# Kernel optimization log

Hardware: AMD Instinct MI355X
Metric: run time of the kernel (lower is better)

## Reference

```python
import jax, jax.numpy as jnp
import numpy as np
import math

N = 512; D = 256; L = 6; H = 8; BINS = 64; LAM = 30.0; STEPS = 8; VOCAB = 20


def _pe(n, d):
    pos = jnp.arange(n, dtype=jnp.float32)[:, None]
    div = jnp.exp(jnp.arange(0, d, 2, dtype=jnp.float32) * (-math.log(10000.0) / d))
    pe = jnp.zeros((n, d), jnp.float32)
    pe = pe.at[:, 0::2].set(jnp.sin(pos * div))
    pe = pe.at[:, 1::2].set(jnp.cos(pos * div))
    return pe


def _ln(x, g, b, eps=1e-5):
    m = x.mean(-1, keepdims=True)
    v = x.var(-1, keepdims=True)
    return (x - m) / jnp.sqrt(v + eps) * g + b


def _gelu(x):
    return jax.nn.gelu(x, approximate=False)  # torch nn.GELU default (erf)


def setup_inputs() -> dict:
    key = jax.random.key(0)
    ks = jax.random.split(key, 20)
    s = 0.02
    nrm = lambda k, sh: jax.random.normal(k, sh, jnp.float32) * s
    z = lambda sh: jnp.zeros(sh, jnp.float32)
    o = lambda sh: jnp.ones(sh, jnp.float32)
    return {
        "tokens": jax.random.randint(ks[0], (1, N), 0, VOCAB),
        "emb": nrm(ks[1], (VOCAB, D)),
        "Wqkv": nrm(ks[2], (L, 3 * D, D)), "bqkv": z((L, 3 * D)),
        "Wo": nrm(ks[3], (L, D, D)), "bo": z((L, D)),
        "g1": o((L, D)), "be1": z((L, D)),
        "W1": nrm(ks[4], (L, 4 * D, D)), "b1": z((L, 4 * D)),
        "W2": nrm(ks[5], (L, D, 4 * D)), "b2": z((L, D)),
        "g2": o((L, D)), "be2": z((L, D)),
        "A1": nrm(ks[6], (D, D)), "a1b": z((D,)),
        "A2": nrm(ks[7], (1, D)), "a2b": z((1,)),
        "Cf": nrm(ks[8], (D, D)), "cb": z((D,)),
        "F1": nrm(ks[9], (D, 2 * D)), "f1b": z((D,)),
        "F2": nrm(ks[10], (BINS, D)), "f2b": z((BINS,)),
        "T1": nrm(ks[11], (D, D)), "t1b": z((D,)),
        "T2": nrm(ks[12], (2, D)), "t2b": z((2,)),
        "Cp": nrm(ks[13], (3, D)), "cpb": z((3,)),
        "noise": jax.random.normal(ks[14], (1, N, 3), jnp.float32),
    }


def reference(tokens, emb, Wqkv, bqkv, Wo, bo, g1, be1, W1, b1, W2, b2, g2, be2,
              A1, a1b, A2, a2b, Cf, cb, F1, f1b, F2, f2b, T1, t1b, T2, t2b,
              Cp, cpb, noise):
    x = emb[tokens] + _pe(N, D)  # [1,N,D]
    dh = D // H
    for l in range(L):  # post-norm TransformerEncoderLayer, ReLU activation
        qkv = x @ Wqkv[l].T + bqkv[l]  # [1,N,3D]
        q, k, v = jnp.split(qkv, 3, axis=-1)
        q = q.reshape(1, N, H, dh).transpose(0, 2, 1, 3)
        k = k.reshape(1, N, H, dh).transpose(0, 2, 1, 3)
        v = v.reshape(1, N, H, dh).transpose(0, 2, 1, 3)
        att = jax.nn.softmax(jnp.einsum('bhqd,bhkd->bhqk', q, k) / math.sqrt(dh), axis=-1)
        o = jnp.einsum('bhqk,bhkd->bhqd', att, v).transpose(0, 2, 1, 3).reshape(1, N, D)
        x = _ln(x + o @ Wo[l].T + bo[l], g1[l], be1[l])
        f = jax.nn.relu(x @ W1[l].T + b1[l]) @ W2[l].T + b2[l]
        x = _ln(x + f, g2[l], be2[l])
    latent = x
    # AdaptiveAlphaPredictor
    ah = _gelu(latent @ A1.T + a1b) @ A2.T + a2b  # [1,N,1]
    alpha = 1.2 + jax.nn.sigmoid(ah)[..., 0] * (3.5 - 1.2)  # [1,N]
    # CSOCRGAttention: power-law x exp-decay kernel over |i-j|
    idx = jnp.arange(N, dtype=jnp.float32)
    r = jnp.abs(idx[:, None] - idx[None, :]) + 1e-4  # [N,N]
    ap = (alpha[:, :, None] + alpha[:, None, :]) * 0.5  # [1,N,N]
    kern = r[None] ** (-ap) * jnp.exp(-r[None] / LAM)
    kern = kern / (kern.sum(-1, keepdims=True) + 1e-8)
    latent = jnp.einsum('bij,bjd->bid', kern, latent)
    # ContactPriorHead
    hh = latent @ Cf.T + cb
    contact = jax.nn.sigmoid(jnp.einsum('bid,bjd->bij', hh, hh))
    # DistogramHead: cat([xi, xj]) @ F1.T == xi @ F1[:, :D].T + xj @ F1[:, D:].T
    hi = latent @ F1[:, :D].T  # [1,N,D]
    hj = latent @ F1[:, D:].T  # [1,N,D]
    ph = _gelu(hi[:, :, None, :] + hj[:, None, :, :] + f1b)  # [1,N,N,D]
    disto = ph @ F2.T + f2b  # [1,N,N,BINS]
    # TorsionGenerator
    t = _gelu(latent @ T1.T + t1b) @ T2.T + t2b  # [1,N,2]
    phi = jnp.tanh(t[..., 0]) * jnp.pi
    psi = jnp.tanh(t[..., 1]) * jnp.pi
    # DiffusionInitializer: fixed small sequential refinement loop
    target = latent @ Cp.T + cpb  # [1,N,3]
    xc = noise
    for tt in reversed(range(STEPS)):
        a = (tt + 1) / STEPS
        xc = a * xc + (1.0 - a) * target
    return latent, alpha, contact, disto, phi, psi, xc


if __name__ == "__main__":
    outs = reference(**setup_inputs())
    for o in outs:
        print(o.shape, o.dtype)
```

## Files before the change

kernel.cpp:

```cpp
#include <hip/hip_runtime.h>
#include <hip/hip_bf16.h>

#define DEV __device__ __forceinline__

typedef float f32x4 __attribute__((ext_vector_type(4)));
typedef short short8 __attribute__((ext_vector_type(8)));
typedef short short4v __attribute__((ext_vector_type(4)));

#if __has_builtin(__builtin_amdgcn_exp2f)
#define EXP2F __builtin_amdgcn_exp2f
#else
#define EXP2F exp2f
#endif
#if __has_builtin(__builtin_amdgcn_rcpf)
#define RCPF __builtin_amdgcn_rcpf
#else
#define RCPF(x) (1.f / (x))
#endif

DEV short f2bf(float f) {
    union { float f; unsigned u; } c; c.f = f;
    unsigned r = (c.u + 0x7FFFu + ((c.u >> 16) & 1u)) >> 16;
    return (short)r;
}

DEV int cvt_pk_bf16(float lo, float hi) {
    int d;
    asm("v_cvt_pk_bf16_f32 %0, %1, %2" : "=v"(d) : "v"(lo), "v"(hi));
    return d;
}

DEV float gelu_fast(float x) {
    float x2 = x * x;
    float y = x * __builtin_fmaf(0.0356774081f, x2, 0.7978845608f);
    y = fminf(fmaxf(y, -15.f), 15.f);
    float e = EXP2F(y * 2.8853900817779268f);
    float r = RCPF(e + 1.f);
    float t = (e - 1.f) * r;
    return 0.5f * x * (1.f + t);
}

DEV float wred_sum(float v) {
    #pragma unroll
    for (int off = 1; off < 64; off <<= 1) v += __shfl_xor(v, off);
    return v;
}

struct CvtPack {
    const float* s[9];
    short* d[9];
    int n[9];
};
__global__ __launch_bounds__(256) void k_cvt_all(CvtPack p) {
    #pragma unroll 1
    for (int seg = 0; seg < 9; ++seg) {
        int n4 = p.n[seg] >> 2;
        const float4* src = (const float4*)p.s[seg];
        short4v* dst = (short4v*)p.d[seg];
        for (int i = blockIdx.x * 256 + threadIdx.x; i < n4; i += gridDim.x * 256) {
            float4 v = src[i];
            short4v o;
            o[0] = f2bf(v.x); o[1] = f2bf(v.y); o[2] = f2bf(v.z); o[3] = f2bf(v.w);
            dst[i] = o;
        }
    }
}

__global__ __launch_bounds__(256) void k_embed(const int* __restrict__ tokens,
                                               const float* __restrict__ emb,
                                               float* __restrict__ x,
                                               short* __restrict__ xb) {
    int n = blockIdx.x, d = threadIdx.x;
    int tok = tokens[n];
    float div = expf((float)((d >> 1) * 2) * -0.035977892079030837f);
    float arg = (float)n * div;
    float pe = (d & 1) ? cosf(arg) : sinf(arg);
    float v = emb[tok * 256 + d] + pe;
    x[n * 256 + d] = v;
    xb[n * 256 + d] = f2bf(v);
}

__global__ __launch_bounds__(64) void k_gemm16(const short* __restrict__ A,
                                               const short* __restrict__ W,
                                               const float* __restrict__ bias,
                                               float* __restrict__ outf,
                                               short* __restrict__ outb,
                                               short* __restrict__ vt,
                                               int M, int K, int ldw, int act) {
    int m0 = blockIdx.x * 16, n0 = blockIdx.y * 16;
    int lane = threadIdx.x;
    int cr = lane & 15, g = lane >> 4;
    const short* a0 = A + (size_t)(n0 + cr) * K + g * 8;
    const short* b0 = W + (size_t)(m0 + cr) * ldw + g * 8;
    f32x4 acc = {0.f, 0.f, 0.f, 0.f};
    #pragma unroll 8
    for (int k = 0; k < K; k += 32) {
        short8 av = *(const short8*)(a0 + k);
        short8 bv = *(const short8*)(b0 + k);
        acc = __builtin_amdgcn_mfma_f32_16x16x32_bf16(av, bv, acc, 0, 0, 0);
    }
    float bb = bias ? bias[m0 + cr] : 0.f;
    int m = m0 + cr;
    #pragma unroll
    for (int r = 0; r < 4; ++r) {
        int row = n0 + g * 4 + r;
        float v = acc[r] + bb;
        if (act == 1) v = fmaxf(v, 0.f);
        else if (act == 2) v = gelu_fast(v);
        else if (act == 3) v = 1.f / (1.f + __expf(-v));
        if (outf) outf[(size_t)row * M + m] = v;
        if (outb) outb[(size_t)row * M + m] = f2bf(v);
        if (vt && m >= 512) vt[(size_t)(m - 512) * 512 + row] = f2bf(v);
    }
}

__global__ __launch_bounds__(64) void k_attn3(const short* __restrict__ qkvb,
                                              const short* __restrict__ vt,
                                              short* __restrict__ obuf_bf) {
    __shared__ __align__(16) short Pb[16][40];
    int h = blockIdx.x, qt = blockIdx.y;
    int lane = threadIdx.x;
    int cr = lane & 15, g = lane >> 4;
    int qb = qt * 16;
    short8 qf = *(const short8*)(qkvb + (size_t)(qb + cr) * 768 + h * 32 + g * 8);
    f32x4 s[32];
    #pragma unroll
    for (int jt = 0; jt < 32; ++jt) {
        short8 kf = *(const short8*)(qkvb + (size_t)(jt * 16 + cr) * 768 + 256 + h * 32 + g * 8);
        f32x4 z = {0.f, 0.f, 0.f, 0.f};
        s[jt] = __builtin_amdgcn_mfma_f32_16x16x32_bf16(qf, kf, z, 0, 0, 0);
    }
    const float sc = 0.17677669529663687f;
    float m[4], l[4];
    #pragma unroll
    for (int r = 0; r < 4; ++r) {
        float mm = -1e30f;
        #pragma unroll
        for (int jt = 0; jt < 32; ++jt) mm = fmaxf(mm, s[jt][r]);
        #pragma unroll
        for (int off = 1; off < 16; off <<= 1) mm = fmaxf(mm, __shfl_xor(mm, off));
        m[r] = mm * sc;
    }
    #pragma unroll
    for (int r = 0; r < 4; ++r) {
        float ll = 0.f;
        #pragma unroll
        for (int jt = 0; jt < 32; ++jt) {
            float p = __expf(s[jt][r] * sc - m[r]);
            s[jt][r] = p;
            ll += p;
        }
        #pragma unroll
        for (int off = 1; off < 16; off <<= 1) ll += __shfl_xor(ll, off);
        l[r] = ll;
    }
    const short* vth0 = vt + (size_t)(h * 32 + cr) * 512;
    const short* vth1 = vt + (size_t)(h * 32 + 16 + cr) * 512;
    f32x4 o0 = {0.f,0.f,0.f,0.f}, o1 = o0;
    #pragma unroll
    for (int c = 0; c < 16; ++c) {
        #pragma unroll
        for (int r = 0; r < 4; ++r) {
            Pb[4 * g + r][cr]      = f2bf(s[2 * c][r]);
            Pb[4 * g + r][16 + cr] = f2bf(s[2 * c + 1][r]);
        }
        short8 pa = *(const short8*)&Pb[cr][g * 8];
        short8 v0 = *(const short8*)(vth0 + c * 32 + g * 8);
        short8 v1 = *(const short8*)(vth1 + c * 32 + g * 8);
        o0 = __builtin_amdgcn_mfma_f32_16x16x32_bf16(pa, v0, o0, 0, 0, 0);
        o1 = __builtin_amdgcn_mfma_f32_16x16x32_bf16(pa, v1, o1, 0, 0, 0);
    }
    #pragma unroll
    for (int r = 0; r < 4; ++r) {
        float inv = 1.f / l[r];
        int q = qb + 4 * g + r;
        short* op = obuf_bf + (size_t)q * 256 + h * 32;
        op[cr]      = f2bf(o0[r] * inv);
        op[16 + cr] = f2bf(o1[r] * inv);
    }
}

__global__ __launch_bounds__(64) void k_ln(const float* xr, const float* y,
                                           const float* __restrict__ g,
                                           const float* __restrict__ b,
                                           float* out, short* outb) {
    int n = blockIdx.x, lane = threadIdx.x;
    float4 xv = *(const float4*)(xr + (size_t)n * 256 + lane * 4);
    float4 yv = *(const float4*)(y + (size_t)n * 256 + lane * 4);
    float t0 = xv.x + yv.x, t1 = xv.y + yv.y, t2 = xv.z + yv.z, t3 = xv.w + yv.w;
    float s = t0 + t1 + t2 + t3;
    float sq = t0 * t0 + t1 * t1 + t2 * t2 + t3 * t3;
    s = wred_sum(s);
    sq = wred_sum(sq);
    float mean = s * (1.f / 256.f);
    float var = sq * (1.f / 256.f) - mean * mean;
    float rstd = rsqrtf(var + 1e-5f);
    float4 gv = *(const float4*)(g + lane * 4);
    float4 bv = *(const float4*)(b + lane * 4);
    float r0 = (t0 - mean) * rstd * gv.x + bv.x;
    float r1 = (t1 - mean) * rstd * gv.y + bv.y;
    float r2 = (t2 - mean) * rstd * gv.z + bv.z;
    float r3 = (t3 - mean) * rstd * gv.w + bv.w;
    *(float4*)(out + (size_t)n * 256 + lane * 4) = make_float4(r0, r1, r2, r3);
    short4v ob; ob[0] = f2bf(r0); ob[1] = f2bf(r1); ob[2] = f2bf(r2); ob[3] = f2bf(r3);
    *(short4v*)(outb + (size_t)n * 256 + lane * 4) = ob;
}

__global__ __launch_bounds__(64) void k_alpha(const float* __restrict__ g,
                                              const float* __restrict__ A2,
                                              const float* __restrict__ a2b,
                                              float* __restrict__ alpha) {
    int n = blockIdx.x, lane = threadIdx.x;
    float4 gv = *(const float4*)(g + (size_t)n * 256 + lane * 4);
    float4 av = *(const float4*)(A2 + lane * 4);
    float s = gv.x * av.x + gv.y * av.y + gv.z * av.z + gv.w * av.w;
    s = wred_sum(s);
    if (lane == 0) {
        float ah = s + a2b[0];
        alpha[n] = 1.2f + 2.3f / (1.f + __expf(-ah));
    }
}

__global__ __launch_bounds__(256) void k_kern(const float* __restrict__ latent,
                                              const float* __restrict__ alpha,
                                              float* __restrict__ out,
                                              short* __restrict__ outb) {
    __shared__ float wl[512];
    __shared__ float partial[4];
    int i = blockIdx.x, t = threadIdx.x;
    float ai = alpha[i];
    float w0, w1;
    {
        int j = t;
        float dd = fabsf((float)(i - j)) + 1e-4f;
        float ap = 0.5f * (ai + alpha[j]);
        w0 = exp2f(-ap * __log2f(dd) - dd * 0.048089834696298776f);
        j = t + 256;
        dd = fabsf((float)(i - j)) + 1e-4f;
        ap = 0.5f * (ai + alpha[j]);
        w1 = exp2f(-ap * __log2f(dd) - dd * 0.048089834696298776f);
    }
    wl[t] = w0; wl[t + 256] = w1;
    float s = wred_sum(w0 + w1);
    if ((t & 63) == 0) partial[t >> 6] = s;
    __syncthreads();
    float S = partial[0] + partial[1] + partial[2] + partial[3];
    float inv = 1.f / (S + 1e-8f);
    float acc = 0.f;
    #pragma unroll 4
    for (int j = 0; j < 512; ++j) acc += wl[j] * latent[(size_t)j * 256 + t];
    float v = acc * inv;
    out[(size_t)i * 256 + t] = v;
    outb[(size_t)i * 256 + t] = f2bf(v);
}

__global__ __launch_bounds__(256) void k_disto4(const float* __restrict__ hi,
                                                const float* __restrict__ hj,
                                                const short* __restrict__ F2bf,
                                                const float* __restrict__ f2b,
                                                float* __restrict__ out) {
    __shared__ __align__(16) float hjs[16][260];
    int jt = blockIdx.x, it = blockIdx.y;
    int j0 = jt * 16;
    int t = threadIdx.x;
    for (int q = t; q < 1024; q += 256) {
        int r = q >> 6, c = (q & 63) << 2;
        *(float4*)&hjs[r][c] = *(const float4*)(hj + (size_t)(j0 + r) * 256 + c);
    }
    __syncthreads();
    int w = t >> 6, lane = t & 63;
    int cr = lane & 15, g = lane >> 4;
    int i0 = it * 8 + w * 2;
    float bb[4];
    #pragma unroll
    for (int c = 0; c < 4; ++c) bb[c] = f2b[c * 16 + cr];
    f32x4 acc[2][4];
    #pragma unroll
    for (int ii = 0; ii < 2; ++ii)
        #pragma unroll
        for (int c = 0; c < 4; ++c) acc[ii][c] = (f32x4){0.f,0.f,0.f,0.f};
    #pragma unroll 1
    for (int ks = 0; ks < 8; ++ks) {
        int kb = ks * 32 + g * 8;
        short8 B[4];
        #pragma unroll
        for (int c = 0; c < 4; ++c)
            B[c] = *(const short8*)(F2bf + (size_t)(c * 16 + cr) * 256 + kb);
        float4 ja = *(const float4*)&hjs[cr][kb];
        float4 jb = *(const float4*)&hjs[cr][kb + 4];
        #pragma unroll
        for (int ii = 0; ii < 2; ++ii) {
            const float* hr = hi + (size_t)(i0 + ii) * 256 + kb;
            float4 ha = *(const float4*)(hr);
            float4 hb = *(const float4*)(hr + 4);
            float p0 = gelu_fast(ha.x + ja.x);
            float p1 = gelu_fast(ha.y + ja.y);
            float p2 = gelu_fast(ha.z + ja.z);
            float p3 = gelu_fast(ha.w + ja.w);
            float p4 = gelu_fast(hb.x + jb.x);
            float p5 = gelu_fast(hb.y + jb.y);
            float p6 = gelu_fast(hb.z + jb.z);
            float p7 = gelu_fast(hb.w + jb.w);
            union { int i[4]; short8 s; } u;
            u.i[0] = cvt_pk_bf16(p0, p1);
            u.i[1] = cvt_pk_bf16(p2, p3);
            u.i[2] = cvt_pk_bf16(p4, p5);
            u.i[3] = cvt_pk_bf16(p6, p7);
            #pragma unroll
            for (int c = 0; c < 4; ++c)
                acc[ii][c] = __builtin_amdgcn_mfma_f32_16x16x32_bf16(u.s, B[c], acc[ii][c], 0, 0, 0);
        }
    }
    #pragma unroll
    for (int ii = 0; ii < 2; ++ii) {
        #pragma unroll
        for (int r = 0; r < 4; ++r) {
            int jl = g * 4 + r;
            float* op = out + ((size_t)(i0 + ii) * 512 + j0 + jl) * 64;
            op[cr]      = acc[ii][0][r] + bb[0];
            op[cr + 16] = acc[ii][1][r] + bb[1];
            op[cr + 32] = acc[ii][2][r] + bb[2];
            op[cr + 48] = acc[ii][3][r] + bb[3];
        }
    }
}

__global__ __launch_bounds__(64) void k_torsion(const float* __restrict__ g,
                                                const float* __restrict__ T2,
                                                const float* __restrict__ t2b,
                                                float* __restrict__ phi,
                                                float* __restrict__ psi) {
    int n = blockIdx.x, lane = threadIdx.x;
    float4 gv = *(const float4*)(g + (size_t)n * 256 + lane * 4);
    float4 w0 = *(const float4*)(T2 + lane * 4);
    float4 w1 = *(const float4*)(T2 + 256 + lane * 4);
    float s0 = gv.x * w0.x + gv.y * w0.y + gv.z * w0.z + gv.w * w0.w;
    float s1 = gv.x * w1.x + gv.y * w1.y + gv.z * w1.z + gv.w * w1.w;
    s0 = wred_sum(s0);
    s1 = wred_sum(s1);
    if (lane == 0) {
        phi[n] = tanhf(s0 + t2b[0]) * 3.14159265358979323846f;
        psi[n] = tanhf(s1 + t2b[1]) * 3.14159265358979323846f;
    }
}

__global__ __launch_bounds__(64) void k_diffusion(const float* __restrict__ latent,
                                                  const float* __restrict__ Cp,
                                                  const float* __restrict__ cpb,
                                                  const float* __restrict__ noise,
                                                  float* __restrict__ xc) {
    int n = blockIdx.x, lane = threadIdx.x;
    float4 lv = *(const float4*)(latent + (size_t)n * 256 + lane * 4);
    const float CN = 40320.0f / 16777216.0f;
    float s[3];
    #pragma unroll
    for (int c = 0; c < 3; ++c) {
        float4 w = *(const float4*)(Cp + c * 256 + lane * 4);
        float v = lv.x * w.x + lv.y * w.y + lv.z * w.z + lv.w * w.w;
        s[c] = wred_sum(v);
    }
    if (lane == 0) {
        #pragma unroll
        for (int c = 0; c < 3; ++c) {
            float tg = s[c] + cpb[c];
            xc[n * 3 + c] = CN * noise[n * 3 + c] + (1.f - CN) * tg;
        }
    }
}

extern "C" void kernel_launch(void* const* d_in, const int* in_sizes, int n_in,
                              void* d_out, int out_size, void* d_ws, size_t ws_size,
                              hipStream_t stream) {
    const int*   tokens = (const int*)d_in[0];
    const float* emb  = (const float*)d_in[1];
    const float* Wqkv = (const float*)d_in[2];
    const float* bqkv = (const float*)d_in[3];
    const float* Wo   = (const float*)d_in[4];
    const float* bo   = (const float*)d_in[5];
    const float* g1   = (const float*)d_in[6];
    const float* be1  = (const float*)d_in[7];
    const float* W1   = (const float*)d_in[8];
    const float* b1   = (const float*)d_in[9];
    const float* W2   = (const float*)d_in[10];
    const float* b2   = (const float*)d_in[11];
    const float* g2   = (const float*)d_in[12];
    const float* be2  = (const float*)d_in[13];
    const float* A1   = (const float*)d_in[14];
    const float* a1b  = (const float*)d_in[15];
    const float* A2   = (const float*)d_in[16];
    const float* a2b  = (const float*)d_in[17];
    const float* Cf   = (const float*)d_in[18];
    const float* cb   = (const float*)d_in[19];
    const float* F1   = (const float*)d_in[20];
    const float* f1b  = (const float*)d_in[21];
    const float* F2   = (const float*)d_in[22];
    const float* f2b  = (const float*)d_in[23];
    const float* T1   = (const float*)d_in[24];
    const float* t1b  = (const float*)d_in[25];
    const float* T2   = (const float*)d_in[26];
    const float* t2b  = (const float*)d_in[27];
    const float* Cp   = (const float*)d_in[28];
    const float* cpb  = (const float*)d_in[29];
    const float* noise= (const float*)d_in[30];

    float* ws   = (float*)d_ws;
    float* x    = ws;
    float* y2   = ws + 131072;
    float* gbuf = ws + 262144;
    float* hi   = ws + 393216;
    float* hj   = ws + 524288;
    short* S    = (short*)(ws + 655360);
    short* x_bf    = S;
    short* obuf_bf = S + 131072;
    short* h1_bf   = S + 262144;
    short* hh_bf   = S + 786432;
    short* lat_bf  = S + 917504;
    short* F2bf    = S + 1048576;
    short* qkv_bf  = S + 1064960;
    short* vt      = S + 1458176;
    short* Wqkv_bf = S + 1589248;
    short* Wo_bf   = S + 2768896;
    short* W1_bf   = S + 3162112;
    short* W2_bf   = S + 4734976;
    short* A1_bf   = S + 6307840;
    short* Cf_bf   = S + 6373376;
    short* F1_bf   = S + 6438912;
    short* T1_bf   = S + 6569984;

    float* out = (float*)d_out;
    float* o_latent  = out;
    float* o_alpha   = out + 131072;
    float* o_contact = out + 131584;
    float* o_disto   = out + 393728;
    float* o_phi     = out + 17170944;
    float* o_psi     = out + 17171456;
    float* o_xc      = out + 17171968;

    CvtPack p;
    p.s[0] = Wqkv; p.d[0] = Wqkv_bf; p.n[0] = 1179648;
    p.s[1] = Wo;   p.d[1] = Wo_bf;   p.n[1] = 393216;
    p.s[2] = W1;   p.d[2] = W1_bf;   p.n[2] = 1572864;
    p.s[3] = W2;   p.d[3] = W2_bf;   p.n[3] = 1572864;
    p.s[4] = A1;   p.d[4] = A1_bf;   p.n[4] = 65536;
    p.s[5] = Cf;   p.d[5] = Cf_bf;   p.n[5] = 65536;
    p.s[6] = F1;   p.d[6] = F1_bf;   p.n[6] = 131072;
    p.s[7] = T1;   p.d[7] = T1_bf;   p.n[7] = 65536;
    p.s[8] = F2;   p.d[8] = F2bf;    p.n[8] = 16384;
    k_cvt_all<<<512, 256, 0, stream>>>(p);

    k_embed<<<512, 256, 0, stream>>>(tokens, emb, x, x_bf);

    for (int l = 0; l < 6; ++l) {
        k_gemm16<<<dim3(48, 32), 64, 0, stream>>>(x_bf, Wqkv_bf + (size_t)l * 196608,
            bqkv + l * 768, nullptr, qkv_bf, vt, 768, 256, 256, 0);
        k_attn3<<<dim3(8, 32), 64, 0, stream>>>(qkv_bf, vt, obuf_bf);
        k_gemm16<<<dim3(16, 32), 64, 0, stream>>>(obuf_bf, Wo_bf + (size_t)l * 65536,
            bo + l * 256, y2, nullptr, nullptr, 256, 256, 256, 0);
        k_ln<<<512, 64, 0, stream>>>(x, y2, g1 + l * 256, be1 + l * 256, x, x_bf);
        k_gemm16<<<dim3(64, 32), 64, 0, stream>>>(x_bf, W1_bf + (size_t)l * 262144,
            b1 + l * 1024, nullptr, h1_bf, nullptr, 1024, 256, 256, 1);
        k_gemm16<<<dim3(16, 32), 64, 0, stream>>>(h1_bf, W2_bf + (size_t)l * 262144,
            b2 + l * 256, y2, nullptr, nullptr, 256, 1024, 1024, 0);
        k_ln<<<512, 64, 0, stream>>>(x, y2, g2 + l * 256, be2 + l * 256, x, x_bf);
    }

    k_gemm16<<<dim3(16, 32), 64, 0, stream>>>(x_bf, A1_bf, a1b, gbuf, nullptr, nullptr,
                                              256, 256, 256, 2);
    k_alpha<<<512, 64, 0, stream>>>(gbuf, A2, a2b, o_alpha);
    k_kern<<<512, 256, 0, stream>>>(x, o_alpha, o_latent, lat_bf);
    k_gemm16<<<dim3(16, 32), 64, 0, stream>>>(lat_bf, Cf_bf, cb, nullptr, hh_bf, nullptr,
                                              256, 256, 256, 0);
    k_gemm16<<<dim3(32, 32), 64, 0, stream>>>(hh_bf, hh_bf, nullptr, o_contact, nullptr,
                                              nullptr, 512, 256, 256, 3);
    k_gemm16<<<dim3(16, 32), 64, 0, stream>>>(lat_bf, F1_bf, f1b, hi, nullptr, nullptr,
                                              256, 256, 512, 0);
    k_gemm16<<<dim3(16, 32), 64, 0, stream>>>(lat_bf, F1_bf + 256, nullptr, hj, nullptr,
                                              nullptr, 256, 256, 512, 0);
    k_disto4<<<dim3(32, 64), 256, 0, stream>>>(hi, hj, F2bf, f2b, o_disto);
    k_gemm16<<<dim3(16, 32), 64, 0, stream>>>(lat_bf, T1_bf, t1b, gbuf, nullptr, nullptr,
                                              256, 256, 256, 2);
    k_torsion<<<512, 64, 0, stream>>>(gbuf, T2, t2b, o_phi, o_psi);
    k_diffusion<<<512, 64, 0, stream>>>(o_latent, Cp, cpb, noise, o_xc);
}
```

Before: 376.9 us.

## Fuse residual adds and LayerNorms into GEMM epilogues and FFN1 prologue

The Wo GEMM now adds the residual in its epilogue. The first LayerNorm is recomputed inside a new FFN1 kernel that normalizes fp32 rows in registers before the MFMA. Both LayerNorms are then applied together in one dual-LN kernel after the W2 GEMM, replacing the two separate per-layer LN launches. This removes one launch and one fp32 round trip per layer, but each FFN1 block now recomputes the LN statistics for its 16 rows, which is redundant work across the 64 column tiles. Separately, the distogram k-loop is now fully unrolled.

```diff
diff --git a/kernel.cpp b/kernel.cpp
--- a/kernel.cpp
+++ b/kernel.cpp
@@ -83,6 +83,7 @@
 __global__ __launch_bounds__(64) void k_gemm16(const short* __restrict__ A,
                                                const short* __restrict__ W,
                                                const float* __restrict__ bias,
+                                               const float* __restrict__ resf,
                                                float* __restrict__ outf,
                                                short* __restrict__ outb,
                                                short* __restrict__ vt,
@@ -105,6 +106,7 @@
     for (int r = 0; r < 4; ++r) {
         int row = n0 + g * 4 + r;
         float v = acc[r] + bb;
+        if (resf) v += resf[(size_t)row * M + m];
         if (act == 1) v = fmaxf(v, 0.f);
         else if (act == 2) v = gelu_fast(v);
         else if (act == 3) v = 1.f / (1.f + __expf(-v));
@@ -112,6 +114,114 @@
         if (outb) outb[(size_t)row * M + m] = f2bf(v);
         if (vt && m >= 512) vt[(size_t)(m - 512) * 512 + row] = f2bf(v);
     }
+}
+
+__global__ __launch_bounds__(64) void k_ffn1(const float* __restrict__ y2,
+                                             const float* __restrict__ gam,
+                                             const float* __restrict__ bet,
+                                             const short* __restrict__ W1,
+                                             const float* __restrict__ b1,
+                                             short* __restrict__ h1) {
+    int m0 = blockIdx.x * 16, n0 = blockIdx.y * 16;
+    int lane = threadIdx.x;
+    int cr = lane & 15, g = lane >> 4;
+    const float* arow = y2 + (size_t)(n0 + cr) * 256 + g * 8;
+    float av[64];
+    float sum = 0.f, sq = 0.f;
+    #pragma unroll
+    for (int ki = 0; ki < 8; ++ki) {
+        float4 a0 = *(const float4*)(arow + ki * 32);
+        float4 a1 = *(const float4*)(arow + ki * 32 + 4);
+        av[ki*8+0]=a0.x; av[ki*8+1]=a0.y; av[ki*8+2]=a0.z; av[ki*8+3]=a0.w;
+        av[ki*8+4]=a1.x; av[ki*8+5]=a1.y; av[ki*8+6]=a1.z; av[ki*8+7]=a1.w;
+        sum += a0.x + a0.y + a0.z + a0.w + a1.x + a1.y + a1.z + a1.w;
+        sq  += a0.x*a0.x + a0.y*a0.y + a0.z*a0.z + a0.w*a0.w
+             + a1.x*a1.x + a1.y*a1.y + a1.z*a1.z + a1.w*a1.w;
+    }
+    sum += __shfl_xor(sum, 16); sum += __shfl_xor(sum, 32);
+    sq  += __shfl_xor(sq, 16);  sq  += __shfl_xor(sq, 32);
+    float mean = sum * (1.f / 256.f);
+    float var = sq * (1.f / 256.f) - mean * mean;
+    float rstd = rsqrtf(var + 1e-5f);
+    short8 afr[8];
+    #pragma unroll
+    for (int ki = 0; ki < 8; ++ki) {
+        int col = ki * 32 + g * 8;
+        float4 g0 = *(const float4*)(gam + col);
+        float4 g1v = *(const float4*)(gam + col + 4);
+        float4 b0 = *(const float4*)(bet + col);
+        float4 b1v = *(const float4*)(bet + col + 4);
+        float v0 = (av[ki*8+0] - mean) * rstd * g0.x + b0.x;
+        float v1 = (av[ki*8+1] - mean) * rstd * g0.y + b0.y;
+        float v2 = (av[ki*8+2] - mean) * rstd * g0.z + b0.z;
+        float v3 = (av[ki*8+3] - mean) * rstd * g0.w + b0.w;
+        float v4 = (av[ki*8+4] - mean) * rstd * g1v.x + b1v.x;
+        float v5 = (av[ki*8+5] - mean) * rstd * g1v.y + b1v.y;
+        float v6 = (av[ki*8+6] - mean) * rstd * g1v.z + b1v.z;
+        float v7 = (av[ki*8+7] - mean) * rstd * g1v.w + b1v.w;
+        union { int i[4]; short8 s; } u;
+        u.i[0] = cvt_pk_bf16(v0, v1);
+        u.i[1] = cvt_pk_bf16(v2, v3);
+        u.i[2] = cvt_pk_bf16(v4, v5);
+        u.i[3] = cvt_pk_bf16(v6, v7);
+        afr[ki] = u.s;
+    }
+    const short* b0p = W1 + (size_t)(m0 + cr) * 256 + g * 8;
+    f32x4 acc = {0.f, 0.f, 0.f, 0.f};
+    #pragma unroll
+    for (int ki = 0; ki < 8; ++ki) {
+        short8 bv = *(const short8*)(b0p + ki * 32);
+        acc = __builtin_amdgcn_mfma_f32_16x16x32_bf16(afr[ki], bv, acc, 0, 0, 0);
+    }
+    float bb = b1[m0 + cr];
+    int m = m0 + cr;
+    #pragma unroll
+    for (int r = 0; r < 4; ++r) {
+        int row = n0 + g * 4 + r;
+        h1[(size_t)row * 1024 + m] = f2bf(fmaxf(acc[r] + bb, 0.f));
+    }
+}
+
+__global__ __launch_bounds__(64) void k_ln_dual(const float* __restrict__ yA,
+                                                const float* __restrict__ yB,
+                                                const float* __restrict__ g1,
+                                                const float* __restrict__ be1,
+                                                const float* __restrict__ g2,
+                                                const float* __restrict__ be2,
+                                                float* __restrict__ out,
+                                                short* __restrict__ outb) {
+    int n = blockIdx.x, lane = threadIdx.x;
+    float4 a = *(const float4*)(yA + (size_t)n * 256 + lane * 4);
+    float s = a.x + a.y + a.z + a.w;
+    float q = a.x*a.x + a.y*a.y + a.z*a.z + a.w*a.w;
+    s = wred_sum(s);
+    q = wred_sum(q);
+    float mean1 = s * (1.f / 256.f);
+    float var1 = q * (1.f / 256.f) - mean1 * mean1;
+    float rstd1 = rsqrtf(var1 + 1e-5f);
+    float4 g1v = *(const float4*)(g1 + lane * 4);
+    float4 b1v = *(const float4*)(be1 + lane * 4);
+    float4 b = *(const float4*)(yB + (size_t)n * 256 + lane * 4);
+    float t0 = (a.x - mean1) * rstd1 * g1v.x + b1v.x + b.x;
+    float t1 = (a.y - mean1) * rstd1 * g1v.y + b1v.y + b.y;
+    float t2 = (a.z - mean1) * rstd1 * g1v.z + b1v.z + b.z;
+    float t3 = (a.w - mean1) * rstd1 * g1v.w + b1v.w + b.w;
+    float s2 = t0 + t1 + t2 + t3;
+    float q2 = t0*t0 + t1*t1 + t2*t2 + t3*t3;
+    s2 = wred_sum(s2);
+    q2 = wred_sum(q2);
+    float mean2 = s2 * (1.f / 256.f);
+    float var2 = q2 * (1.f / 256.f) - mean2 * mean2;
+    float rstd2 = rsqrtf(var2 + 1e-5f);
+    float4 g2v = *(const float4*)(g2 + lane * 4);
+    float4 b2v = *(const float4*)(be2 + lane * 4);
+    float r0 = (t0 - mean2) * rstd2 * g2v.x + b2v.x;
+    float r1 = (t1 - mean2) * rstd2 * g2v.y + b2v.y;
+    float r2 = (t2 - mean2) * rstd2 * g2v.z + b2v.z;
+    float r3 = (t3 - mean2) * rstd2 * g2v.w + b2v.w;
+    *(float4*)(out + (size_t)n * 256 + lane * 4) = make_float4(r0, r1, r2, r3);
+    short4v ob; ob[0] = f2bf(r0); ob[1] = f2bf(r1); ob[2] = f2bf(r2); ob[3] = f2bf(r3);
+    *(short4v*)(outb + (size_t)n * 256 + lane * 4) = ob;
 }
 
 __global__ __launch_bounds__(64) void k_attn3(const short* __restrict__ qkvb,
@@ -178,32 +288,6 @@
         op[cr]      = f2bf(o0[r] * inv);
         op[16 + cr] = f2bf(o1[r] * inv);
     }
-}
-
-__global__ __launch_bounds__(64) void k_ln(const float* xr, const float* y,
-                                           const float* __restrict__ g,
-                                           const float* __restrict__ b,
-                                           float* out, short* outb) {
-    int n = blockIdx.x, lane = threadIdx.x;
-    float4 xv = *(const float4*)(xr + (size_t)n * 256 + lane * 4);
-    float4 yv = *(const float4*)(y + (size_t)n * 256 + lane * 4);
-    float t0 = xv.x + yv.x, t1 = xv.y + yv.y, t2 = xv.z + yv.z, t3 = xv.w + yv.w;
-    float s = t0 + t1 + t2 + t3;
-    float sq = t0 * t0 + t1 * t1 + t2 * t2 + t3 * t3;
-    s = wred_sum(s);
-    sq = wred_sum(sq);
-    float mean = s * (1.f / 256.f);
-    float var = sq * (1.f / 256.f) - mean * mean;
-    float rstd = rsqrtf(var + 1e-5f);
-    float4 gv = *(const float4*)(g + lane * 4);
-    float4 bv = *(const float4*)(b + lane * 4);
-    float r0 = (t0 - mean) * rstd * gv.x + bv.x;
-    float r1 = (t1 - mean) * rstd * gv.y + bv.y;
-    float r2 = (t2 - mean) * rstd * gv.z + bv.z;
-    float r3 = (t3 - mean) * rstd * gv.w + bv.w;
-    *(float4*)(out + (size_t)n * 256 + lane * 4) = make_float4(r0, r1, r2, r3);
-    short4v ob; ob[0] = f2bf(r0); ob[1] = f2bf(r1); ob[2] = f2bf(r2); ob[3] = f2bf(r3);
-    *(short4v*)(outb + (size_t)n * 256 + lane * 4) = ob;
 }
 
 __global__ __launch_bounds__(64) void k_alpha(const float* __restrict__ g,
@@ -254,11 +338,11 @@
     outb[(size_t)i * 256 + t] = f2bf(v);
 }
 
-__global__ __launch_bounds__(256) void k_disto4(const float* __restrict__ hi,
-                                                const float* __restrict__ hj,
-                                                const short* __restrict__ F2bf,
-                                                const float* __restrict__ f2b,
-                                                float* __restrict__ out) {
+__global__ __launch_bounds__(256) void k_disto4b(const float* __restrict__ hi,
+                                                 const float* __restrict__ hj,
+                                                 const short* __restrict__ F2bf,
+                                                 const float* __restrict__ f2b,
+                                                 float* __restrict__ out) {
     __shared__ __align__(16) float hjs[16][260];
     int jt = blockIdx.x, it = blockIdx.y;
     int j0 = jt * 16;
@@ -279,7 +363,7 @@
     for (int ii = 0; ii < 2; ++ii)
         #pragma unroll
         for (int c = 0; c < 4; ++c) acc[ii][c] = (f32x4){0.f,0.f,0.f,0.f};
-    #pragma unroll 1
+    #pragma unroll
     for (int ks = 0; ks < 8; ++ks) {
         int kb = ks * 32 + g * 8;
         short8 B[4];
@@ -406,10 +490,11 @@
     float* ws   = (float*)d_ws;
     float* x    = ws;
     float* y2   = ws + 131072;
-    float* gbuf = ws + 262144;
-    float* hi   = ws + 393216;
-    float* hj   = ws + 524288;
-    short* S    = (short*)(ws + 655360);
+    float* y3   = ws + 262144;
+    float* gbuf = ws + 393216;
+    float* hi   = ws + 524288;
+    float* hj   = ws + 655360;
+    short* S    = (short*)(ws + 786432);
     short* x_bf    = S;
     short* obuf_bf = S + 131072;
     short* h1_bf   = S + 262144;
@@ -452,33 +537,33 @@
 
     for (int l = 0; l < 6; ++l) {
         k_gemm16<<<dim3(48, 32), 64, 0, stream>>>(x_bf, Wqkv_bf + (size_t)l * 196608,
-            bqkv + l * 768, nullptr, qkv_bf, vt, 768, 256, 256, 0);
+            bqkv + l * 768, nullptr, nullptr, qkv_bf, vt, 768, 256, 256, 0);
         k_attn3<<<dim3(8, 32), 64, 0, stream>>>(qkv_bf, vt, obuf_bf);
         k_gemm16<<<dim3(16, 32), 64, 0, stream>>>(obuf_bf, Wo_bf + (size_t)l * 65536,
-            bo + l * 256, y2, nullptr, nullptr, 256, 256, 256, 0);
-        k_ln<<<512, 64, 0, stream>>>(x, y2, g1 + l * 256, be1 + l * 256, x, x_bf);
-        k_gemm16<<<dim3(64, 32), 64, 0, stream>>>(x_bf, W1_bf + (size_t)l * 262144,
-            b1 + l * 1024, nullptr, h1_bf, nullptr, 1024, 256, 256, 1);
+            bo + l * 256, x, y2, nullptr, nullptr, 256, 256, 256, 0);
+        k_ffn1<<<dim3(64, 32), 64, 0, stream>>>(y2, g1 + l * 256, be1 + l * 256,
+            W1_bf + (size_t)l * 262144, b1 + l * 1024, h1_bf);
         k_gemm16<<<dim3(16, 32), 64, 0, stream>>>(h1_bf, W2_bf + (size_t)l * 262144,
-            b2 + l * 256, y2, nullptr, nullptr, 256, 1024, 1024, 0);
-        k_ln<<<512, 64, 0, stream>>>(x, y2, g2 + l * 256, be2 + l * 256, x, x_bf);
-    }
-
-    k_gemm16<<<dim3(16, 32), 64, 0, stream>>>(x_bf, A1_bf, a1b, gbuf, nullptr, nullptr,
-                                              256, 256, 256, 2);
+            b2 + l * 256, nullptr, y3, nullptr, nullptr, 256, 1024, 1024, 0);
+        k_ln_dual<<<512, 64, 0, stream>>>(y2, y3, g1 + l * 256, be1 + l * 256,
+                                          g2 + l * 256, be2 + l * 256, x, x_bf);
+    }
+
+    k_gemm16<<<dim3(16, 32), 64, 0, stream>>>(x_bf, A1_bf, a1b, nullptr, gbuf, nullptr,
+                                              nullptr, 256, 256, 256, 2);
     k_alpha<<<512, 64, 0, stream>>>(gbuf, A2, a2b, o_alpha);
     k_kern<<<512, 256, 0, stream>>>(x, o_alpha, o_latent, lat_bf);
-    k_gemm16<<<dim3(16, 32), 64, 0, stream>>>(lat_bf, Cf_bf, cb, nullptr, hh_bf, nullptr,
-                                              256, 256, 256, 0);
-    k_gemm16<<<dim3(32, 32), 64, 0, stream>>>(hh_bf, hh_bf, nullptr, o_contact, nullptr,
-                                              nullptr, 512, 256, 256, 3);
-    k_gemm16<<<dim3(16, 32), 64, 0, stream>>>(lat_bf, F1_bf, f1b, hi, nullptr, nullptr,
-                                              256, 256, 512, 0);
-    k_gemm16<<<dim3(16, 32), 64, 0, stream>>>(lat_bf, F1_bf + 256, nullptr, hj, nullptr,
+    k_gemm16<<<dim3(16, 32), 64, 0, stream>>>(lat_bf, Cf_bf, cb, nullptr, nullptr, hh_bf,
+                                              nullptr, 256, 256, 256, 0);
+    k_gemm16<<<dim3(32, 32), 64, 0, stream>>>(hh_bf, hh_bf, nullptr, nullptr, o_contact,
+                                              nullptr, nullptr, 512, 256, 256, 3);
+    k_gemm16<<<dim3(16, 32), 64, 0, stream>>>(lat_bf, F1_bf, f1b, nullptr, hi, nullptr,
                                               nullptr, 256, 256, 512, 0);
-    k_disto4<<<dim3(32, 64), 256, 0, stream>>>(hi, hj, F2bf, f2b, o_disto);
-    k_gemm16<<<dim3(16, 32), 64, 0, stream>>>(lat_bf, T1_bf, t1b, gbuf, nullptr, nullptr,
-                                              256, 256, 256, 2);
+    k_gemm16<<<dim3(16, 32), 64, 0, stream>>>(lat_bf, F1_bf + 256, nullptr, nullptr, hj,
+                                              nullptr, nullptr, 256, 256, 512, 0);
+    k_disto4b<<<dim3(32, 64), 256, 0, stream>>>(hi, hj, F2bf, f2b, o_disto);
+    k_gemm16<<<dim3(16, 32), 64, 0, stream>>>(lat_bf, T1_bf, t1b, nullptr, gbuf, nullptr,
+                                              nullptr, 256, 256, 256, 2);
     k_torsion<<<512, 64, 0, stream>>>(gbuf, T2, t2b, o_phi, o_psi);
     k_diffusion<<<512, 64, 0, stream>>>(o_latent, Cp, cpb, noise, o_xc);
 }
```

Measured after the change: 392.2 us. 4.1% more time.
